# Kernel tuning notes

Measured on AMD Instinct MI355X. Metric: run time of the kernel, lower is better.

The kernel has to match this reference:

```python
import jax, jax.numpy as jnp
import numpy as np

MAX_LENGTH = 256
WIDTH = 4


def _attention_matrix(a, b):
    # a, b: (B, M, D) with M = max_length + width - 1
    # euclidean match score: 1 / (1 + ||a_i - b_j||_2)
    sq = (
        jnp.sum(a * a, axis=-1)[:, :, None]
        + jnp.sum(b * b, axis=-1)[:, None, :]
        - 2.0 * jnp.einsum('bid,bjd->bij', a, b)
    )
    dist = jnp.sqrt(jnp.maximum(sq, 0.0))
    return 1.0 / (1.0 + dist)  # (B, M, M)


def reference(x1, x2):
    # x1, x2: (B, 1, M, D), M = MAX_LENGTH + WIDTH - 1
    a = x1[:, 0]  # (B, M, D)
    b = x2[:, 0]
    A = _attention_matrix(a, b)  # (B, M, M), A[b,i,j] = score(a_i, b_j)
    # row_sum over dim i of A[:,:,k] weights x1 column k; col analogously for x2.
    w_a = jnp.sum(A, axis=1)  # (B, M): sum_i A[i, k]
    w_b = jnp.sum(A, axis=2)  # (B, M): sum_j A[k, j]
    y1 = w_a[:, :, None] * a  # (B, M, D)
    y2 = w_b[:, :, None] * b
    # sliding-window sum of width WIDTH: w[j] = sum_{k=j}^{j+WIDTH-1} y[k]
    w1 = sum(y1[:, d:d + MAX_LENGTH, :] for d in range(WIDTH))
    w2 = sum(y2[:, d:d + MAX_LENGTH, :] for d in range(WIDTH))
    return (w1[:, None], w2[:, None])  # (B, 1, MAX_LENGTH, D) each


def setup_inputs() -> dict:
    key = jax.random.key(0)
    k1, k2 = jax.random.split(key)
    B, M, D = 128, MAX_LENGTH + WIDTH - 1, 512
    x1 = jax.random.normal(k1, (B, 1, M, D), dtype=jnp.float32)
    x2 = jax.random.normal(k2, (B, 1, M, D), dtype=jnp.float32)
    return {"x1": x1, "x2": x2}
```

## Files before the change

kernel.cpp:

```cpp
#include <hip/hip_runtime.h>

#define BATCH 128
#define M 259
#define D 512
#define T 256
#define NM (BATCH * M)
#define OUTHALF (BATCH * T * D)

typedef __bf16 bf16;
typedef __bf16 bf16x4 __attribute__((ext_vector_type(4)));
typedef __bf16 bf16x8 __attribute__((ext_vector_type(8)));
typedef float f32x4 __attribute__((ext_vector_type(4)));


__global__ void k_zero(float4* __restrict__ ws4) {
    int i = blockIdx.x * 256 + threadIdx.x;
    if (i < (2 * NM + 3) / 4) ws4[i] = make_float4(0.f, 0.f, 0.f, 0.f);
}

#define BT 96
#define BK 64
#define NTL 3

__launch_bounds__(256)
__global__ void k_pairs(const float* __restrict__ x1, const float* __restrict__ x2,
                        float* __restrict__ ws) {
    __shared__ __align__(16) bf16 As[BT * BK];
    __shared__ __align__(16) bf16 Bs[BT * BK];
    __shared__ float na_s[BT];
    __shared__ float nb_s[BT];

    int s   = blockIdx.x;
    int bid = (s & 7) * 144 + (s >> 3);
    int b   = bid / 9;
    int ti  = (bid % 9) / 3;
    int tj  = bid % 3;
    int i0  = ti * BT, j0 = tj * BT;

    int t    = threadIdx.x;
    int lane = t & 63;
    int w    = t >> 6;
    int wm   = w >> 1, wn = w & 1;
    int iw   = i0 + wm * 48;
    int jw   = j0 + wn * 48;

    const float* Ab = x1 + (size_t)b * M * D;
    const float* Bb = x2 + (size_t)b * M * D;

    const float* pa[6];
    const float* pb[6];
    int c4 = (t & 15) * 4;
#pragma unroll
    for (int p = 0; p < 6; ++p) {
        int ra = min(i0 + p * 16 + (t >> 4), M - 1);
        int rb = min(j0 + p * 16 + (t >> 4), M - 1);
        pa[p] = Ab + (size_t)ra * D + c4;
        pb[p] = Bb + (size_t)rb * D + c4;
    }
    int wslot   = (t & 15) >> 1;
    int wwithin = (t & 1) * 4;
    int wr_off[6];
#pragma unroll
    for (int p = 0; p < 6; ++p) {
        int row = p * 16 + (t >> 4);
        wr_off[p] = row * BK + ((wslot ^ (row & 7)) << 3) + wwithin;
    }

    int a_off[3][2], b_off[3][2];
#pragma unroll
    for (int fm = 0; fm < 3; ++fm) {
        int rowa = wm * 48 + fm * 16 + (lane & 15);
        int rowb = wn * 48 + fm * 16 + (lane & 15);
#pragma unroll
        for (int kk = 0; kk < 2; ++kk) {
            int slot = kk * 4 + (lane >> 4);
            a_off[fm][kk] = rowa * BK + ((slot ^ (rowa & 7)) << 3);
            b_off[fm][kk] = rowb * BK + ((slot ^ (rowb & 7)) << 3);
        }
    }

    f32x4 acc[3][3];
#pragma unroll
    for (int fm = 0; fm < 3; ++fm)
#pragma unroll
        for (int fn = 0; fn < 3; ++fn) acc[fm][fn] = (f32x4)0.f;

    float sa[6], sb[6];
#pragma unroll
    for (int p = 0; p < 6; ++p) { sa[p] = 0.f; sb[p] = 0.f; }

    for (int k0 = 0; k0 < D; k0 += BK) {
        float4 va[6], vb[6];
#pragma unroll
        for (int p = 0; p < 6; ++p) {
            va[p] = *(const float4*)(pa[p] + k0);
            vb[p] = *(const float4*)(pb[p] + k0);
        }
#pragma unroll
        for (int p = 0; p < 6; ++p) {
            sa[p] += va[p].x * va[p].x + va[p].y * va[p].y
                   + va[p].z * va[p].z + va[p].w * va[p].w;
            sb[p] += vb[p].x * vb[p].x + vb[p].y * vb[p].y
                   + vb[p].z * vb[p].z + vb[p].w * vb[p].w;
        }
        __syncthreads();
#pragma unroll
        for (int p = 0; p < 6; ++p) {
            bf16x4 ca = { (bf16)va[p].x, (bf16)va[p].y, (bf16)va[p].z, (bf16)va[p].w };
            bf16x4 cb = { (bf16)vb[p].x, (bf16)vb[p].y, (bf16)vb[p].z, (bf16)vb[p].w };
            *(bf16x4*)&As[wr_off[p]] = ca;
            *(bf16x4*)&Bs[wr_off[p]] = cb;
        }
        __syncthreads();
#pragma unroll
        for (int kk = 0; kk < 2; ++kk) {
            bf16x8 af[3], bfr[3];
#pragma unroll
            for (int fm = 0; fm < 3; ++fm) af[fm]  = *(const bf16x8*)&As[a_off[fm][kk]];
#pragma unroll
            for (int fn = 0; fn < 3; ++fn) bfr[fn] = *(const bf16x8*)&Bs[b_off[fn][kk]];
#pragma unroll
            for (int fm = 0; fm < 3; ++fm)
#pragma unroll
                for (int fn = 0; fn < 3; ++fn)
                    acc[fm][fn] = __builtin_amdgcn_mfma_f32_16x16x32_bf16(
                        af[fm], bfr[fn], acc[fm][fn], 0, 0, 0);
        }
    }

#pragma unroll
    for (int p = 0; p < 6; ++p) {
        float v1 = sa[p], v2 = sb[p];
        v1 += __shfl_xor(v1, 1); v1 += __shfl_xor(v1, 2);
        v1 += __shfl_xor(v1, 4); v1 += __shfl_xor(v1, 8);
        v2 += __shfl_xor(v2, 1); v2 += __shfl_xor(v2, 2);
        v2 += __shfl_xor(v2, 4); v2 += __shfl_xor(v2, 8);
        if ((t & 15) == 0) {
            na_s[p * 16 + (t >> 4)] = v1;
            nb_s[p * 16 + (t >> 4)] = v2;
        }
    }
    __syncthreads();

    int b_off_w = b * M;
    float na_[3][4], nb_[3];
#pragma unroll
    for (int fm = 0; fm < 3; ++fm)
#pragma unroll
        for (int r = 0; r < 4; ++r)
            na_[fm][r] = na_s[wm * 48 + fm * 16 + (lane >> 4) * 4 + r];
#pragma unroll
    for (int fn = 0; fn < 3; ++fn)
        nb_[fn] = nb_s[wn * 48 + fn * 16 + (lane & 15)];

    float rs[3][4];
    float cs[3];
#pragma unroll
    for (int fm = 0; fm < 3; ++fm)
#pragma unroll
        for (int r = 0; r < 4; ++r) rs[fm][r] = 0.f;
#pragma unroll
    for (int fn = 0; fn < 3; ++fn) cs[fn] = 0.f;

#pragma unroll
    for (int fm = 0; fm < 3; ++fm) {
#pragma unroll
        for (int fn = 0; fn < 3; ++fn) {
#pragma unroll
            for (int r = 0; r < 4; ++r) {
                int i = iw + fm * 16 + (lane >> 4) * 4 + r;
                int j = jw + fn * 16 + (lane & 15);
                float av = 0.f;
                if (i < M && j < M) {
                    float sq   = na_[fm][r] + nb_[fn] - 2.f * acc[fm][fn][r];
                    float dist = sqrtf(fmaxf(sq, 0.f));
                    av = 1.f / (1.f + dist);
                }
                rs[fm][r] += av;
                cs[fn]    += av;
            }
        }
    }

#pragma unroll
    for (int fm = 0; fm < 3; ++fm)
#pragma unroll
        for (int r = 0; r < 4; ++r) {
            float v = rs[fm][r];
            v += __shfl_xor(v, 1); v += __shfl_xor(v, 2);
            v += __shfl_xor(v, 4); v += __shfl_xor(v, 8);
            int i = iw + fm * 16 + (lane >> 4) * 4 + r;
            if ((lane & 15) == 0 && i < M) atomicAdd(&ws[NM + b_off_w + i], v);
        }
#pragma unroll
    for (int fn = 0; fn < 3; ++fn) {
        float v = cs[fn];
        v += __shfl_xor(v, 16); v += __shfl_xor(v, 32);
        int j = jw + fn * 16 + (lane & 15);
        if ((lane >> 4) == 0 && j < M) atomicAdd(&ws[b_off_w + j], v);
    }
}

__global__ void k_out(const float* __restrict__ x1, const float* __restrict__ x2,
                      const float* __restrict__ ws, float* __restrict__ out) {
    int bid   = blockIdx.x;
    int which = bid & 1;
    int tc    = (bid >> 1) & 7;
    int b     = bid >> 4;
    int d4    = threadIdx.x << 2;
    const float* src  = which ? x2 : x1;
    const float* wgt  = ws + (which ? NM : 0) + b * M;
    const float* rows = src + (size_t)b * M * D + d4;
    float* o = out + (size_t)which * OUTHALF + ((size_t)b * T + tc * 32) * D + d4;
    int t0 = tc * 32;
    float4 v0 = *(const float4*)(rows + (size_t)(t0 + 0) * D);
    float4 v1 = *(const float4*)(rows + (size_t)(t0 + 1) * D);
    float4 v2 = *(const float4*)(rows + (size_t)(t0 + 2) * D);
    float s0 = wgt[t0 + 0], s1 = wgt[t0 + 1], s2 = wgt[t0 + 2];
#pragma unroll 4
    for (int tt = 0; tt < 32; ++tt) {
        float4 v3 = *(const float4*)(rows + (size_t)(t0 + tt + 3) * D);
        float s3  = wgt[t0 + tt + 3];
        float4 r;
        r.x = s0 * v0.x + s1 * v1.x + s2 * v2.x + s3 * v3.x;
        r.y = s0 * v0.y + s1 * v1.y + s2 * v2.y + s3 * v3.y;
        r.z = s0 * v0.z + s1 * v1.z + s2 * v2.z + s3 * v3.z;
        r.w = s0 * v0.w + s1 * v1.w + s2 * v2.w + s3 * v3.w;
        *(float4*)(o + (size_t)tt * D) = r;
        v0 = v1; v1 = v2; v2 = v3;
        s0 = s1; s1 = s2; s2 = s3;
    }
}

extern "C" void kernel_launch(void* const* d_in, const int* in_sizes, int n_in,
                              void* d_out, int out_size, void* d_ws, size_t ws_size,
                              hipStream_t stream) {
    const float* x1 = (const float*)d_in[0];
    const float* x2 = (const float*)d_in[1];
    float* out = (float*)d_out;
    float* ws  = (float*)d_ws;

    k_zero<<<(2 * NM / 4 + 255) / 256, 256, 0, stream>>>((float4*)ws);
    k_pairs<<<BATCH * NTL * NTL, 256, 0, stream>>>(x1, x2, ws);
    k_out<<<BATCH * 16, 128, 0, stream>>>(x1, x2, ws, out);
}
```

Baseline: 125.9 us.

## Retile pair kernel to full-row by half-column blocks with shared column sums

The pair-score kernel now launches one 512-thread block per (batch, column half), covering all rows of x1 (padded to 320) against 130 columns of x2. Each block writes its column weights directly after reducing them in shared memory, so the zero-fill kernel clears only the row-weight half. This cuts redundant global loads of x1/x2 tiles (each A row is loaded twice instead of three times) and global atomics, but uses a larger 5x5 MFMA accumulator per wave. Padding rows beyond 259 waste MFMA work, and only 256 blocks are launched, which may underfill the GPU.

```diff
diff --git a/kernel.cpp b/kernel.cpp
--- a/kernel.cpp
+++ b/kernel.cpp
@@ -6,6 +6,10 @@
 #define T 256
 #define NM (BATCH * M)
 #define OUTHALF (BATCH * T * D)
+#define MP 320
+#define HJ 160
+#define PROWS 480
+#define BK 64
 
 typedef __bf16 bf16;
 typedef __bf16 bf16x4 __attribute__((ext_vector_type(4)));
@@ -13,192 +17,171 @@
 typedef float f32x4 __attribute__((ext_vector_type(4)));
 
 
-__global__ void k_zero(float4* __restrict__ ws4) {
+__global__ void k_zero(float* __restrict__ ws) {
     int i = blockIdx.x * 256 + threadIdx.x;
-    if (i < (2 * NM + 3) / 4) ws4[i] = make_float4(0.f, 0.f, 0.f, 0.f);
-}
-
-#define BT 96
-#define BK 64
-#define NTL 3
-
-__launch_bounds__(256)
+    if (i < NM) ws[NM + i] = 0.f;
+}
+
+__launch_bounds__(512)
 __global__ void k_pairs(const float* __restrict__ x1, const float* __restrict__ x2,
                         float* __restrict__ ws) {
-    __shared__ __align__(16) bf16 As[BT * BK];
-    __shared__ __align__(16) bf16 Bs[BT * BK];
-    __shared__ float na_s[BT];
-    __shared__ float nb_s[BT];
-
-    int s   = blockIdx.x;
-    int bid = (s & 7) * 144 + (s >> 3);
-    int b   = bid / 9;
-    int ti  = (bid % 9) / 3;
-    int tj  = bid % 3;
-    int i0  = ti * BT, j0 = tj * BT;
+    __shared__ __align__(16) bf16 P[PROWS * BK];
+    __shared__ float nrm[PROWS];
+    __shared__ float wcol_s[HJ];
+
+    int sblk = blockIdx.x;
+    int bid  = (sblk & 7) * 32 + (sblk >> 3);
+    int b  = bid >> 1;
+    int jh = bid & 1;
+    int j0 = jh * 130;
 
     int t    = threadIdx.x;
     int lane = t & 63;
     int w    = t >> 6;
-    int wm   = w >> 1, wn = w & 1;
-    int iw   = i0 + wm * 48;
-    int jw   = j0 + wn * 48;
+    int wm   = w >> 1;
+    int wn   = w & 1;
 
     const float* Ab = x1 + (size_t)b * M * D;
     const float* Bb = x2 + (size_t)b * M * D;
 
-    const float* pa[6];
-    const float* pb[6];
-    int c4 = (t & 15) * 4;
-#pragma unroll
-    for (int p = 0; p < 6; ++p) {
-        int ra = min(i0 + p * 16 + (t >> 4), M - 1);
-        int rb = min(j0 + p * 16 + (t >> 4), M - 1);
-        pa[p] = Ab + (size_t)ra * D + c4;
-        pb[p] = Bb + (size_t)rb * D + c4;
-    }
-    int wslot   = (t & 15) >> 1;
-    int wwithin = (t & 1) * 4;
-    int wr_off[6];
-#pragma unroll
-    for (int p = 0; p < 6; ++p) {
-        int row = p * 16 + (t >> 4);
-        wr_off[p] = row * BK + ((wslot ^ (row & 7)) << 3) + wwithin;
-    }
-
-    int a_off[3][2], b_off[3][2];
-#pragma unroll
-    for (int fm = 0; fm < 3; ++fm) {
-        int rowa = wm * 48 + fm * 16 + (lane & 15);
-        int rowb = wn * 48 + fm * 16 + (lane & 15);
+    if (t < HJ) wcol_s[t] = 0.f;
+
+    int q = t >> 4, c4f = t & 15;
+    int off[15], wro[15];
+#pragma unroll
+    for (int p = 0; p < 15; ++p) {
+        int row  = q + 32 * p;
+        int grow = (p < 10) ? min(row, M - 1) : min(j0 + (row - MP), M - 1);
+        off[p] = grow * D + c4f * 4;
+        wro[p] = row * BK + (((c4f >> 1) ^ (row & 7)) << 3) + (t & 1) * 4;
+    }
+
+    int a_off[5][2], b_off[5][2];
+#pragma unroll
+    for (int f = 0; f < 5; ++f) {
+        int rowa = wm * 80 + f * 16 + (lane & 15);
+        int rowb = MP + wn * 80 + f * 16 + (lane & 15);
 #pragma unroll
         for (int kk = 0; kk < 2; ++kk) {
             int slot = kk * 4 + (lane >> 4);
-            a_off[fm][kk] = rowa * BK + ((slot ^ (rowa & 7)) << 3);
-            b_off[fm][kk] = rowb * BK + ((slot ^ (rowb & 7)) << 3);
-        }
-    }
-
-    f32x4 acc[3][3];
-#pragma unroll
-    for (int fm = 0; fm < 3; ++fm)
-#pragma unroll
-        for (int fn = 0; fn < 3; ++fn) acc[fm][fn] = (f32x4)0.f;
-
-    float sa[6], sb[6];
-#pragma unroll
-    for (int p = 0; p < 6; ++p) { sa[p] = 0.f; sb[p] = 0.f; }
+            a_off[f][kk] = rowa * BK + ((slot ^ (rowa & 7)) << 3);
+            b_off[f][kk] = rowb * BK + ((slot ^ (rowb & 7)) << 3);
+        }
+    }
+
+    f32x4 acc[5][5];
+#pragma unroll
+    for (int fi = 0; fi < 5; ++fi)
+#pragma unroll
+        for (int fj = 0; fj < 5; ++fj) acc[fi][fj] = (f32x4)0.f;
+
+    float sa[15];
+#pragma unroll
+    for (int p = 0; p < 15; ++p) sa[p] = 0.f;
+
+#define STAGE5(P0, BASE) do {                                                   \
+        float4 v_[5];                                                           \
+        _Pragma("unroll")                                                       \
+        for (int i_ = 0; i_ < 5; ++i_)                                          \
+            v_[i_] = *(const float4*)((BASE) + off[(P0) + i_] + k0);            \
+        _Pragma("unroll")                                                       \
+        for (int i_ = 0; i_ < 5; ++i_) {                                        \
+            sa[(P0) + i_] += v_[i_].x * v_[i_].x + v_[i_].y * v_[i_].y          \
+                           + v_[i_].z * v_[i_].z + v_[i_].w * v_[i_].w;         \
+            *(bf16x4*)&P[wro[(P0) + i_]] = bf16x4{ (bf16)v_[i_].x,              \
+                (bf16)v_[i_].y, (bf16)v_[i_].z, (bf16)v_[i_].w };               \
+        } } while (0)
 
     for (int k0 = 0; k0 < D; k0 += BK) {
-        float4 va[6], vb[6];
-#pragma unroll
-        for (int p = 0; p < 6; ++p) {
-            va[p] = *(const float4*)(pa[p] + k0);
-            vb[p] = *(const float4*)(pb[p] + k0);
-        }
-#pragma unroll
-        for (int p = 0; p < 6; ++p) {
-            sa[p] += va[p].x * va[p].x + va[p].y * va[p].y
-                   + va[p].z * va[p].z + va[p].w * va[p].w;
-            sb[p] += vb[p].x * vb[p].x + vb[p].y * vb[p].y
-                   + vb[p].z * vb[p].z + vb[p].w * vb[p].w;
-        }
         __syncthreads();
-#pragma unroll
-        for (int p = 0; p < 6; ++p) {
-            bf16x4 ca = { (bf16)va[p].x, (bf16)va[p].y, (bf16)va[p].z, (bf16)va[p].w };
-            bf16x4 cb = { (bf16)vb[p].x, (bf16)vb[p].y, (bf16)vb[p].z, (bf16)vb[p].w };
-            *(bf16x4*)&As[wr_off[p]] = ca;
-            *(bf16x4*)&Bs[wr_off[p]] = cb;
-        }
+        STAGE5(0, Ab);
+        STAGE5(5, Ab);
+        STAGE5(10, Bb);
         __syncthreads();
 #pragma unroll
         for (int kk = 0; kk < 2; ++kk) {
-            bf16x8 af[3], bfr[3];
-#pragma unroll
-            for (int fm = 0; fm < 3; ++fm) af[fm]  = *(const bf16x8*)&As[a_off[fm][kk]];
-#pragma unroll
-            for (int fn = 0; fn < 3; ++fn) bfr[fn] = *(const bf16x8*)&Bs[b_off[fn][kk]];
-#pragma unroll
-            for (int fm = 0; fm < 3; ++fm)
-#pragma unroll
-                for (int fn = 0; fn < 3; ++fn)
-                    acc[fm][fn] = __builtin_amdgcn_mfma_f32_16x16x32_bf16(
-                        af[fm], bfr[fn], acc[fm][fn], 0, 0, 0);
-        }
-    }
-
-#pragma unroll
-    for (int p = 0; p < 6; ++p) {
-        float v1 = sa[p], v2 = sb[p];
-        v1 += __shfl_xor(v1, 1); v1 += __shfl_xor(v1, 2);
-        v1 += __shfl_xor(v1, 4); v1 += __shfl_xor(v1, 8);
-        v2 += __shfl_xor(v2, 1); v2 += __shfl_xor(v2, 2);
-        v2 += __shfl_xor(v2, 4); v2 += __shfl_xor(v2, 8);
-        if ((t & 15) == 0) {
-            na_s[p * 16 + (t >> 4)] = v1;
-            nb_s[p * 16 + (t >> 4)] = v2;
-        }
+            bf16x8 af[5], bfr[5];
+#pragma unroll
+            for (int f = 0; f < 5; ++f) af[f]  = *(const bf16x8*)&P[a_off[f][kk]];
+#pragma unroll
+            for (int f = 0; f < 5; ++f) bfr[f] = *(const bf16x8*)&P[b_off[f][kk]];
+#pragma unroll
+            for (int fi = 0; fi < 5; ++fi)
+#pragma unroll
+                for (int fj = 0; fj < 5; ++fj)
+                    acc[fi][fj] = __builtin_amdgcn_mfma_f32_16x16x32_bf16(
+                        af[fi], bfr[fj], acc[fi][fj], 0, 0, 0);
+        }
+    }
+#undef STAGE5
+
+#pragma unroll
+    for (int p = 0; p < 15; ++p) {
+        float v = sa[p];
+        v += __shfl_xor(v, 1); v += __shfl_xor(v, 2);
+        v += __shfl_xor(v, 4); v += __shfl_xor(v, 8);
+        if ((t & 15) == 0) nrm[q + 32 * p] = v;
     }
     __syncthreads();
 
-    int b_off_w = b * M;
-    float na_[3][4], nb_[3];
-#pragma unroll
-    for (int fm = 0; fm < 3; ++fm)
+    float na_[5][4], nb_[5];
+#pragma unroll
+    for (int f = 0; f < 5; ++f) {
 #pragma unroll
         for (int r = 0; r < 4; ++r)
-            na_[fm][r] = na_s[wm * 48 + fm * 16 + (lane >> 4) * 4 + r];
-#pragma unroll
-    for (int fn = 0; fn < 3; ++fn)
-        nb_[fn] = nb_s[wn * 48 + fn * 16 + (lane & 15)];
-
-    float rs[3][4];
-    float cs[3];
-#pragma unroll
-    for (int fm = 0; fm < 3; ++fm)
-#pragma unroll
-        for (int r = 0; r < 4; ++r) rs[fm][r] = 0.f;
-#pragma unroll
-    for (int fn = 0; fn < 3; ++fn) cs[fn] = 0.f;
-
-#pragma unroll
-    for (int fm = 0; fm < 3; ++fm) {
-#pragma unroll
-        for (int fn = 0; fn < 3; ++fn) {
+            na_[f][r] = nrm[wm * 80 + f * 16 + (lane >> 4) * 4 + r];
+        nb_[f] = nrm[MP + wn * 80 + f * 16 + (lane & 15)];
+    }
+
+    float rs[5][4], cs[5];
+#pragma unroll
+    for (int f = 0; f < 5; ++f) {
+#pragma unroll
+        for (int r = 0; r < 4; ++r) rs[f][r] = 0.f;
+        cs[f] = 0.f;
+    }
+
+#pragma unroll
+    for (int fi = 0; fi < 5; ++fi) {
+#pragma unroll
+        for (int fj = 0; fj < 5; ++fj) {
 #pragma unroll
             for (int r = 0; r < 4; ++r) {
-                int i = iw + fm * 16 + (lane >> 4) * 4 + r;
-                int j = jw + fn * 16 + (lane & 15);
+                int i  = wm * 80 + fi * 16 + (lane >> 4) * 4 + r;
+                int lj = wn * 80 + fj * 16 + (lane & 15);
+                int jg = j0 + lj;
                 float av = 0.f;
-                if (i < M && j < M) {
-                    float sq   = na_[fm][r] + nb_[fn] - 2.f * acc[fm][fn][r];
+                if (i < M && lj < 130 && jg < M) {
+                    float sq   = na_[fi][r] + nb_[fj] - 2.f * acc[fi][fj][r];
                     float dist = sqrtf(fmaxf(sq, 0.f));
                     av = 1.f / (1.f + dist);
                 }
-                rs[fm][r] += av;
-                cs[fn]    += av;
+                rs[fi][r] += av;
+                cs[fj]    += av;
             }
         }
     }
 
-#pragma unroll
-    for (int fm = 0; fm < 3; ++fm)
+    int b_off_w = b * M;
+#pragma unroll
+    for (int f = 0; f < 5; ++f)
 #pragma unroll
         for (int r = 0; r < 4; ++r) {
-            float v = rs[fm][r];
+            float v = rs[f][r];
             v += __shfl_xor(v, 1); v += __shfl_xor(v, 2);
             v += __shfl_xor(v, 4); v += __shfl_xor(v, 8);
-            int i = iw + fm * 16 + (lane >> 4) * 4 + r;
+            int i = wm * 80 + f * 16 + (lane >> 4) * 4 + r;
             if ((lane & 15) == 0 && i < M) atomicAdd(&ws[NM + b_off_w + i], v);
         }
 #pragma unroll
-    for (int fn = 0; fn < 3; ++fn) {
-        float v = cs[fn];
+    for (int f = 0; f < 5; ++f) {
+        float v = cs[f];
         v += __shfl_xor(v, 16); v += __shfl_xor(v, 32);
-        int j = jw + fn * 16 + (lane & 15);
-        if ((lane >> 4) == 0 && j < M) atomicAdd(&ws[b_off_w + j], v);
-    }
+        if ((lane >> 4) == 0)
+            atomicAdd(&wcol_s[wn * 80 + f * 16 + (lane & 15)], v);
+    }
+    __syncthreads();
+    if (t < HJ && t < 130 && j0 + t < M) ws[b_off_w + j0 + t] = wcol_s[t];
 }
 
 __global__ void k_out(const float* __restrict__ x1, const float* __restrict__ x2,
@@ -240,7 +223,7 @@
     float* out = (float*)d_out;
     float* ws  = (float*)d_ws;
 
-    k_zero<<<(2 * NM / 4 + 255) / 256, 256, 0, stream>>>((float4*)ws);
-    k_pairs<<<BATCH * NTL * NTL, 256, 0, stream>>>(x1, x2, ws);
+    k_zero<<<(NM + 255) / 256, 256, 0, stream>>>(ws);
+    k_pairs<<<256, 512, 0, stream>>>(x1, x2, ws);
     k_out<<<BATCH * 16, 128, 0, stream>>>(x1, x2, ws, out);
 }
```

After: 103.8 us (median of 2 runs). 1.21x faster.
